# Kernel tuning notes

Measured on AMD Instinct MI355X. Metric: run time of the kernel, lower is better.

## Reference

```python
import jax, jax.numpy as jnp
import numpy as np

NEG_SLOPE = 0.2

def gatv2_layer(x, src, dst, Wl, bl, Wr, br, att, bias, N, concat):
    # Wl/Wr: [F_in, H*C]; att: [H, C]
    H, C = att.shape
    xl = (x @ Wl + bl).reshape(-1, H, C)  # source transform [N,H,C]
    xr = (x @ Wr + br).reshape(-1, H, C)  # target transform [N,H,C]
    e = jax.nn.leaky_relu(xl[src] + xr[dst], NEG_SLOPE)          # [E,H,C]
    logits = jnp.einsum('ehc,hc->eh', e, att)                    # [E,H]
    m = jax.ops.segment_max(logits, dst, num_segments=N)         # [N,H]
    p = jnp.exp(logits - m[dst])
    s = jax.ops.segment_sum(p, dst, num_segments=N)              # [N,H]
    alpha = p / s[dst]                                           # [E,H] softmax per dst
    out = jax.ops.segment_sum(alpha[:, :, None] * xl[src], dst, num_segments=N)  # [N,H,C]
    out = out.reshape(N, H * C) if concat else out.mean(axis=1)
    return out + bias


def setup_inputs() -> dict:
    key = jax.random.key(0)
    N, E, F_in = 50000, 500000, 58
    ks = jax.random.split(key, 16)
    s = 0.1
    inp = {
        'x': jax.random.normal(ks[0], (N, F_in), jnp.float32),
        'edge_index': jax.random.randint(ks[1], (2, E), 0, N, jnp.int64),
        'Wl1': jax.random.normal(ks[2], (F_in, 256), jnp.float32) * s,
        'bl1': jnp.zeros((256,), jnp.float32),
        'Wr1': jax.random.normal(ks[3], (F_in, 256), jnp.float32) * s,
        'br1': jnp.zeros((256,), jnp.float32),
        'att1': jax.random.normal(ks[4], (4, 64), jnp.float32) * s,
        'bias1': jnp.zeros((256,), jnp.float32),
        'Wl2': jax.random.normal(ks[5], (256, 256), jnp.float32) * s,
        'bl2': jnp.zeros((256,), jnp.float32),
        'Wr2': jax.random.normal(ks[6], (256, 256), jnp.float32) * s,
        'br2': jnp.zeros((256,), jnp.float32),
        'att2': jax.random.normal(ks[7], (4, 64), jnp.float32) * s,
        'bias2': jnp.zeros((256,), jnp.float32),
        'Wl3': jax.random.normal(ks[8], (256, 6), jnp.float32) * s,
        'bl3': jnp.zeros((6,), jnp.float32),
        'Wr3': jax.random.normal(ks[9], (256, 6), jnp.float32) * s,
        'br3': jnp.zeros((6,), jnp.float32),
        'att3': jax.random.normal(ks[10], (6, 1), jnp.float32) * s,
        'bias3': jnp.zeros((1,), jnp.float32),
    }
    return inp


def reference(x, edge_index, Wl1, bl1, Wr1, br1, att1, bias1,
              Wl2, bl2, Wr2, br2, att2, bias2,
              Wl3, bl3, Wr3, br3, att3, bias3):
    N = x.shape[0]
    loop = jnp.arange(N, dtype=edge_index.dtype)
    src = jnp.concatenate([edge_index[0], loop])  # self-loops (PyG default)
    dst = jnp.concatenate([edge_index[1], loop])
    h = jax.nn.elu(gatv2_layer(x, src, dst, Wl1, bl1, Wr1, br1, att1, bias1, N, True))
    h = jax.nn.elu(gatv2_layer(h, src, dst, Wl2, bl2, Wr2, br2, att2, bias2, N, True))
    out = gatv2_layer(h, src, dst, Wl3, bl3, Wr3, br3, att3, bias3, N, False)
    return out  # [N, 1]
```

## Files before the change

### kernel.cpp

```cpp
#include <hip/hip_runtime.h>
#include <math.h>

#define NEG_SLOPE 0.2f
#define LOG2E 1.4426950408889634f

typedef __attribute__((ext_vector_type(2))) _Float16 h2;
typedef __attribute__((ext_vector_type(4))) _Float16 h4;
typedef __attribute__((ext_vector_type(8))) _Float16 f16x8;
typedef __attribute__((ext_vector_type(4))) float f32x4;

template<int CTRL>
__device__ __forceinline__ float dpp_add_f32(float x) {
    int y = __builtin_amdgcn_update_dpp(0, __float_as_int(x), CTRL, 0xF, 0xF, true);
    return x + __int_as_float(y);
}
__device__ __forceinline__ float rowsum16(float x) {
    x = dpp_add_f32<0xB1>(x);
    x = dpp_add_f32<0x4E>(x);
    x = dpp_add_f32<0x124>(x);
    x = dpp_add_f32<0x128>(x);
    return x;
}


__global__ __launch_bounds__(256) void k_count(const int* __restrict__ ei, int E, int Et,
                                               int* __restrict__ cnt) {
    int e = blockIdx.x * 256 + threadIdx.x;
    if (e < Et) {
        int d = (e < E) ? ei[E + e] : (e - E);
        atomicAdd(&cnt[d], 1);
    }
}

__global__ __launch_bounds__(256) void k_scan_block(const int* __restrict__ cnt,
                                                    int* __restrict__ out,
                                                    int* __restrict__ bsums, int n) {
    __shared__ int tmp[256];
    int t = threadIdx.x;
    int i = blockIdx.x * 256 + t;
    int v = (i < n) ? cnt[i] : 0;
    tmp[t] = v;
    __syncthreads();
    for (int d = 1; d < 256; d <<= 1) {
        int add = (t >= d) ? tmp[t - d] : 0;
        __syncthreads();
        tmp[t] += add;
        __syncthreads();
    }
    if (i < n) out[i] = tmp[t] - v;
    if (t == 255) bsums[blockIdx.x] = tmp[t];
}

__global__ __launch_bounds__(256) void k_scan_bsums(int* bsums, int nb) {
    __shared__ int tmp[256];
    int t = threadIdx.x;
    int v = (t < nb) ? bsums[t] : 0;
    tmp[t] = v;
    __syncthreads();
    for (int d = 1; d < 256; d <<= 1) {
        int add = (t >= d) ? tmp[t - d] : 0;
        __syncthreads();
        tmp[t] += add;
        __syncthreads();
    }
    if (t < nb) bsums[t] = tmp[t] - v;
}

__global__ __launch_bounds__(256) void k_scan_add(int* __restrict__ out,
                                                  const int* __restrict__ bsums,
                                                  int* __restrict__ cursor,
                                                  int n, int total) {
    int i = blockIdx.x * 256 + threadIdx.x;
    if (i < n) {
        int v = out[i] + bsums[blockIdx.x];
        out[i] = v;
        cursor[i] = v;
    }
    if (i == 0) out[n] = total;
}

__global__ __launch_bounds__(256) void k_scatter(const int* __restrict__ ei, int E, int Et,
                                                 int* __restrict__ cursor,
                                                 int* __restrict__ src_sorted) {
    int e = blockIdx.x * 256 + threadIdx.x;
    if (e < Et) {
        int s, d;
        if (e < E) { s = ei[e]; d = ei[E + e]; } else { s = d = e - E; }
        int pos = atomicAdd(&cursor[d], 1);
        src_sorted[pos] = s;
    }
}


__global__ __launch_bounds__(256) void k_cast_x(const float* __restrict__ x,
                                                _Float16* __restrict__ xb,
                                                int N, int F, int kshift) {
    int i = blockIdx.x * 256 + threadIdx.x;
    if (i < (N << kshift)) {
        int n = i >> kshift, k = i & ((1 << kshift) - 1);
        float v = (k < F) ? x[n * F + k] : 0.0f;
        xb[i] = (_Float16)v;
    }
}

__global__ __launch_bounds__(256) void k_cast_w_all(
        const float* __restrict__ Wl1, const float* __restrict__ Wr1,
        const float* __restrict__ Wl2, const float* __restrict__ Wr2,
        const float* __restrict__ Wl3, const float* __restrict__ Wr3,
        _Float16* __restrict__ wtl1, _Float16* __restrict__ wtr1,
        _Float16* __restrict__ wtl2, _Float16* __restrict__ wtr2,
        _Float16* __restrict__ w3t, int F) {
    int i = blockIdx.x * 256 + threadIdx.x;
    if (i < 32768) {
        const float* W = (i < 16384) ? Wl1 : Wr1;
        _Float16* O = (i < 16384) ? wtl1 : wtr1;
        int loc = i & 16383;
        int n = loc >> 6, k = loc & 63;
        O[loc] = (_Float16)(k < F ? W[k * 256 + n] : 0.0f);
    } else if (i < 163840) {
        int seg = i - 32768;
        const float* W = (seg < 65536) ? Wl2 : Wr2;
        _Float16* O = (seg < 65536) ? wtl2 : wtr2;
        int loc = seg & 65535;
        int n = loc >> 8, k = loc & 255;
        O[loc] = (_Float16)W[k * 256 + n];
    } else if (i < 167936) {
        int loc = i - 163840;
        int j = loc >> 8, k = loc & 255;
        float v = (j < 6) ? Wl3[k * 6 + j] : ((j < 12) ? Wr3[k * 6 + (j - 6)] : 0.0f);
        w3t[loc] = (_Float16)v;
    }
}


__global__ __launch_bounds__(256) void k_gemm_pair_mfma(
        const _Float16* __restrict__ A, int M, int Kp,
        const _Float16* __restrict__ Btl, const _Float16* __restrict__ Btr,
        const float* __restrict__ bl, const float* __restrict__ br,
        _Float16* __restrict__ Cl, _Float16* __restrict__ Cr) {
    const int wave = threadIdx.x >> 6, lane = threadIdx.x & 63;
    const int l15 = lane & 15, l4 = lane >> 4;
    const int row0 = blockIdx.x * 64;
    const int mat  = wave >> 1;
    const int col0 = blockIdx.y * 128 + (wave & 1) * 64;
    const _Float16* Bt = mat ? Btr : Btl;
    const float* bias  = mat ? br  : bl;
    _Float16* C        = mat ? Cr  : Cl;

    f32x4 acc[4][4];
    #pragma unroll
    for (int a = 0; a < 4; a++)
        #pragma unroll
        for (int b = 0; b < 4; b++)
            acc[a][b] = (f32x4){0.f, 0.f, 0.f, 0.f};

    int xrow[4];
    #pragma unroll
    for (int nt = 0; nt < 4; nt++) xrow[nt] = min(row0 + nt * 16 + l15, M - 1);
    const _Float16* wbase = Bt + (size_t)(col0 + l15) * Kp + l4 * 8;
    const _Float16* xbase = A + l4 * 8;

    for (int k0 = 0; k0 < Kp; k0 += 32) {
        f16x8 wf[4], xf[4];
        #pragma unroll
        for (int ct = 0; ct < 4; ct++)
            wf[ct] = *(const f16x8*)(wbase + (size_t)(ct * 16) * Kp + k0);
        #pragma unroll
        for (int nt = 0; nt < 4; nt++)
            xf[nt] = *(const f16x8*)(xbase + (size_t)xrow[nt] * Kp + k0);
        #pragma unroll
        for (int ct = 0; ct < 4; ct++)
            #pragma unroll
            for (int nt = 0; nt < 4; nt++)
                acc[ct][nt] = __builtin_amdgcn_mfma_f32_16x16x32_f16(
                    wf[ct], xf[nt], acc[ct][nt], 0, 0, 0);
    }

    float4 bv[4];
    #pragma unroll
    for (int ct = 0; ct < 4; ct++)
        bv[ct] = *(const float4*)&bias[col0 + ct * 16 + l4 * 4];
    #pragma unroll
    for (int nt = 0; nt < 4; nt++) {
        int node = row0 + nt * 16 + l15;
        if (node < M) {
            #pragma unroll
            for (int ct = 0; ct < 4; ct++) {
                h4 hv = {(_Float16)(acc[ct][nt][0] + bv[ct].x),
                         (_Float16)(acc[ct][nt][1] + bv[ct].y),
                         (_Float16)(acc[ct][nt][2] + bv[ct].z),
                         (_Float16)(acc[ct][nt][3] + bv[ct].w)};
                *(h4*)&C[(size_t)node * 256 + col0 + ct * 16 + l4 * 4] = hv;
            }
        }
    }
}


__global__ __launch_bounds__(256) void k_gemm3_mfma(
        const _Float16* __restrict__ h,
        const _Float16* __restrict__ W3t,
        const float* __restrict__ bl, const float* __restrict__ br,
        _Float16* __restrict__ l3, int N) {
    const int wave = threadIdx.x >> 6, lane = threadIdx.x & 63;
    const int l15 = lane & 15, l4 = lane >> 4;
    const int row0 = blockIdx.x * 64 + wave * 16;
    if (row0 >= N) return;

    f16x8 bfr[8];
    #pragma unroll
    for (int ks = 0; ks < 8; ks++)
        bfr[ks] = *(const f16x8*)&W3t[l15 * 256 + ks * 32 + l4 * 8];

    const int arow = min(row0 + l15, N - 1);
    const size_t abase = (size_t)arow * 256;
    f32x4 acc = (f32x4){0.f, 0.f, 0.f, 0.f};
    #pragma unroll
    for (int ks = 0; ks < 8; ks++) {
        f16x8 af = *(const f16x8*)&h[abase + ks * 32 + l4 * 8];
        acc = __builtin_amdgcn_mfma_f32_16x16x32_f16(af, bfr[ks], acc, 0, 0, 0);
    }
    const float bv = (l15 < 6) ? bl[l15] : ((l15 < 12) ? br[l15 - 6] : 0.0f);
    #pragma unroll
    for (int r = 0; r < 4; r++) {
        int gr = row0 + l4 * 4 + r;
        if (gr < N && l15 < 12)
            l3[(size_t)gr * 16 + l15] = (_Float16)(acc[r] + bv);
    }
}


__global__ __launch_bounds__(256) void k_agg256(const _Float16* __restrict__ xl,
                                                const _Float16* __restrict__ xr,
                                                const int* __restrict__ row_ptr,
                                                const int* __restrict__ src_sorted,
                                                const float* __restrict__ att,
                                                const float* __restrict__ bias,
                                                _Float16* __restrict__ h_out, int N) {
    const int wave = threadIdx.x >> 6;
    const int lane = threadIdx.x & 63;
    const int n = __builtin_amdgcn_readfirstlane(blockIdx.x * 4 + wave);
    if (n >= N) return;
    const int ci = lane * 4;
    const h4 xr4 = *(const h4*)&xr[(size_t)n * 256 + ci];
    const float4 at4 = *(const float4*)&att[ci];
    const h2 ata = {(_Float16)(at4.x * LOG2E), (_Float16)(at4.y * LOG2E)};
    const h2 atb = {(_Float16)(at4.z * LOG2E), (_Float16)(at4.w * LOG2E)};
    float a0 = 0.f, a1 = 0.f, a2 = 0.f, a3 = 0.f;
    float m = -INFINITY, s = 0.0f;
    const int beg = row_ptr[n], end = row_ptr[n + 1];

    int j = beg;
    h4 v[8], vn[8];
    bool has = (j + 8 <= end);
    if (has) {
        #pragma unroll
        for (int e = 0; e < 8; e++) {
            int sv = src_sorted[j + e];
            v[e] = *(const h4*)&xl[(size_t)sv * 256 + ci];
        }
    }
    while (has) {
        const int jn = j + 8;
        const bool hasN = (jn + 8 <= end);
        if (hasN) {
            #pragma unroll
            for (int e = 0; e < 8; e++) {
                int sv = src_sorted[jn + e];
                vn[e] = *(const h4*)&xl[(size_t)sv * 256 + ci];
            }
        }
        float lg[8];
        #pragma unroll
        for (int e = 0; e < 8; e++) {
            h4 t = v[e] + xr4;
            h4 lk = __builtin_elementwise_max(t, t * (_Float16)NEG_SLOPE);
            h2 lo = __builtin_shufflevector(lk, lk, 0, 1);
            h2 hi = __builtin_shufflevector(lk, lk, 2, 3);
            lg[e] = __builtin_amdgcn_fdot2(lo, ata,
                        __builtin_amdgcn_fdot2(hi, atb, 0.0f, false), false);
        }
        #pragma unroll
        for (int e = 0; e < 8; e++) lg[e] = rowsum16(lg[e]);
        float bm = fmaxf(fmaxf(fmaxf(lg[0], lg[1]), fmaxf(lg[2], lg[3])),
                         fmaxf(fmaxf(lg[4], lg[5]), fmaxf(lg[6], lg[7])));
        float nm = fmaxf(m, bm);
        float sc = __builtin_amdgcn_exp2f(m - nm);
        a0 *= sc; a1 *= sc; a2 *= sc; a3 *= sc;
        float ps = 0.f;
        #pragma unroll
        for (int e = 0; e < 8; e++) {
            float p = __builtin_amdgcn_exp2f(lg[e] - nm);
            ps += p;
            a0 = fmaf(p, (float)v[e].x, a0);
            a1 = fmaf(p, (float)v[e].y, a1);
            a2 = fmaf(p, (float)v[e].z, a2);
            a3 = fmaf(p, (float)v[e].w, a3);
        }
        s = s * sc + ps;
        m = nm;
        if (hasN) {
            #pragma unroll
            for (int e = 0; e < 8; e++) v[e] = vn[e];
        }
        j = jn;
        has = hasN;
    }
    for (; j < end; j++) {
        int sv = src_sorted[j];
        h4 vv = *(const h4*)&xl[(size_t)sv * 256 + ci];
        h4 t = vv + xr4;
        h4 lk = __builtin_elementwise_max(t, t * (_Float16)NEG_SLOPE);
        h2 lo = __builtin_shufflevector(lk, lk, 0, 1);
        h2 hi = __builtin_shufflevector(lk, lk, 2, 3);
        float lg = __builtin_amdgcn_fdot2(lo, ata,
                       __builtin_amdgcn_fdot2(hi, atb, 0.0f, false), false);
        lg = rowsum16(lg);
        float nm = fmaxf(m, lg);
        float sc = __builtin_amdgcn_exp2f(m - nm);
        float p  = __builtin_amdgcn_exp2f(lg - nm);
        a0 = fmaf(p, (float)vv.x, a0 * sc);
        a1 = fmaf(p, (float)vv.y, a1 * sc);
        a2 = fmaf(p, (float)vv.z, a2 * sc);
        a3 = fmaf(p, (float)vv.w, a3 * sc);
        s = s * sc + p;
        m = nm;
    }
    const float inv = 1.0f / s;
    const float4 bv = *(const float4*)&bias[ci];
    float o0 = a0 * inv + bv.x;
    float o1 = a1 * inv + bv.y;
    float o2 = a2 * inv + bv.z;
    float o3 = a3 * inv + bv.w;
    o0 = o0 > 0.f ? o0 : (__expf(o0) - 1.f);
    o1 = o1 > 0.f ? o1 : (__expf(o1) - 1.f);
    o2 = o2 > 0.f ? o2 : (__expf(o2) - 1.f);
    o3 = o3 > 0.f ? o3 : (__expf(o3) - 1.f);
    h4 hv = {(_Float16)o0, (_Float16)o1, (_Float16)o2, (_Float16)o3};
    *(h4*)&h_out[(size_t)n * 256 + ci] = hv;
}


__global__ __launch_bounds__(64) void k_agg3(const _Float16* __restrict__ l3,
                                             const int* __restrict__ row_ptr,
                                             const int* __restrict__ src_sorted,
                                             const float* __restrict__ att3,
                                             const float* __restrict__ bias3,
                                             float* __restrict__ out, int N) {
    int n = blockIdx.x * 64 + threadIdx.x;
    if (n >= N) return;
    const h4* pn = (const h4*)&l3[(size_t)n * 16];
    h4 q1 = pn[1], q2 = pn[2];
    float xrv[6];
    xrv[0] = (float)q1.z; xrv[1] = (float)q1.w;
    xrv[2] = (float)q2.x; xrv[3] = (float)q2.y;
    xrv[4] = (float)q2.z; xrv[5] = (float)q2.w;
    float attv[6], m[6], s[6], acc[6];
    #pragma unroll
    for (int k = 0; k < 6; k++) {
        attv[k] = att3[k] * LOG2E;
        m[k] = -INFINITY; s[k] = 0.0f; acc[k] = 0.0f;
    }
    int beg = row_ptr[n], end = row_ptr[n + 1];
    for (int idx = beg; idx < end; idx++) {
        int sv = src_sorted[idx];
        const h4* ps = (const h4*)&l3[(size_t)sv * 16];
        h4 u0 = ps[0], u1 = ps[1];
        float xlv[6];
        xlv[0] = (float)u0.x; xlv[1] = (float)u0.y;
        xlv[2] = (float)u0.z; xlv[3] = (float)u0.w;
        xlv[4] = (float)u1.x; xlv[5] = (float)u1.y;
        #pragma unroll
        for (int k = 0; k < 6; k++) {
            float tt = xlv[k] + xrv[k];
            float lr = fmaxf(tt, NEG_SLOPE * tt);
            float logit = attv[k] * lr;
            float nm = fmaxf(m[k], logit);
            float sc = __builtin_amdgcn_exp2f(m[k] - nm);
            float p  = __builtin_amdgcn_exp2f(logit - nm);
            acc[k] = acc[k] * sc + p * xlv[k];
            s[k]   = s[k] * sc + p;
            m[k]   = nm;
        }
    }
    float o = 0.0f;
    #pragma unroll
    for (int k = 0; k < 6; k++) o += acc[k] / s[k];
    out[n] = o * (1.0f / 6.0f) + bias3[0];
}


extern "C" void kernel_launch(void* const* d_in, const int* in_sizes, int n_in,
                              void* d_out, int out_size, void* d_ws, size_t ws_size,
                              hipStream_t stream) {
    const float* x    = (const float*)d_in[0];
    const int*   ei   = (const int*)  d_in[1];
    const float* Wl1  = (const float*)d_in[2];
    const float* bl1  = (const float*)d_in[3];
    const float* Wr1  = (const float*)d_in[4];
    const float* br1  = (const float*)d_in[5];
    const float* att1 = (const float*)d_in[6];
    const float* bias1= (const float*)d_in[7];
    const float* Wl2  = (const float*)d_in[8];
    const float* bl2  = (const float*)d_in[9];
    const float* Wr2  = (const float*)d_in[10];
    const float* br2  = (const float*)d_in[11];
    const float* att2 = (const float*)d_in[12];
    const float* bias2= (const float*)d_in[13];
    const float* Wl3  = (const float*)d_in[14];
    const float* bl3  = (const float*)d_in[15];
    const float* Wr3  = (const float*)d_in[16];
    const float* br3  = (const float*)d_in[17];
    const float* att3 = (const float*)d_in[18];
    const float* bias3= (const float*)d_in[19];

    const int F  = in_sizes[2] / 256;
    const int N  = in_sizes[0] / F;
    const int E  = in_sizes[1] / 2;
    const int Et = E + N;

    char* ws = (char*)d_ws;
    size_t off = 0;
    auto carve = [&](size_t bytes) -> char* {
        char* p = ws + off;
        off = (off + bytes + 255) & ~(size_t)255;
        return p;
    };
    _Float16* xb   = (_Float16*)carve((size_t)N * 64 * 2);
    _Float16* xlb  = (_Float16*)carve((size_t)N * 256 * 2);
    _Float16* xrb  = (_Float16*)carve((size_t)N * 256 * 2);
    _Float16* hb   = (_Float16*)carve((size_t)N * 256 * 2);
    _Float16* wtl1 = (_Float16*)carve(256 * 64 * 2);
    _Float16* wtr1 = (_Float16*)carve(256 * 64 * 2);
    _Float16* wtl2 = (_Float16*)carve(256 * 256 * 2);
    _Float16* wtr2 = (_Float16*)carve(256 * 256 * 2);
    _Float16* w3t  = (_Float16*)carve(16 * 256 * 2);
    _Float16* l3   = (_Float16*)carve((size_t)N * 16 * 2);
    int* cnt        = (int*)carve((size_t)N * 4);
    int* row_ptr    = (int*)carve((size_t)(N + 1) * 4);
    int* cursor     = (int*)carve((size_t)N * 4);
    int* src_sorted = (int*)carve((size_t)Et * 4);
    int* bsums      = (int*)carve(1024 * 4);

    const int gN  = (N + 255) / 256;
    const int gEt = (Et + 255) / 256;
    const int gW  = (N + 3) / 4;

    hipMemsetAsync(cnt, 0, (size_t)N * 4, stream);
    k_count<<<gEt, 256, 0, stream>>>(ei, E, Et, cnt);
    k_scan_block<<<gN, 256, 0, stream>>>(cnt, row_ptr, bsums, N);
    k_scan_bsums<<<1, 256, 0, stream>>>(bsums, gN);
    k_scan_add<<<gN, 256, 0, stream>>>(row_ptr, bsums, cursor, N, Et);
    k_scatter<<<gEt, 256, 0, stream>>>(ei, E, Et, cursor, src_sorted);

    k_cast_x<<<((N << 6) + 255) / 256, 256, 0, stream>>>(x, xb, N, F, 6);
    k_cast_w_all<<<656, 256, 0, stream>>>(Wl1, Wr1, Wl2, Wr2, Wl3, Wr3,
                                          wtl1, wtr1, wtl2, wtr2, w3t, F);

    dim3 gemm_grid((N + 63) / 64, 2);

    k_gemm_pair_mfma<<<gemm_grid, 256, 0, stream>>>(xb, N, 64, wtl1, wtr1, bl1, br1, xlb, xrb);
    k_agg256<<<gW, 256, 0, stream>>>(xlb, xrb, row_ptr, src_sorted, att1, bias1, hb, N);

    k_gemm_pair_mfma<<<gemm_grid, 256, 0, stream>>>(hb, N, 256, wtl2, wtr2, bl2, br2, xlb, xrb);
    k_agg256<<<gW, 256, 0, stream>>>(xlb, xrb, row_ptr, src_sorted, att2, bias2, hb, N);

    k_gemm3_mfma<<<(N + 63) / 64, 256, 0, stream>>>(hb, w3t, bl3, br3, l3, N);
    k_agg3<<<(N + 63) / 64, 64, 0, stream>>>(l3, row_ptr, src_sorted, att3, bias3,
                                             (float*)d_out, N);
}
```

Baseline: 363.8 us.

## Stage GEMM tiles in LDS via global_load_lds with 128x128 block tiles

The paired-projection GEMM now loads 128x32 A and B tiles into shared memory using direct global-to-LDS loads, and each wave reads its fragments from LDS. Each block computes a 128x128 tile of one matrix (grid now 4 in y), so A rows are shared by two waves and B columns by two waves, instead of every wave reading its operands from global memory. It is meant to cut redundant global and L2 traffic in the GEMM. In exchange it adds two barriers per K step with no double buffering, and the LDS fragment reads may hit bank conflicts.

```diff
diff --git a/kernel.cpp b/kernel.cpp
--- a/kernel.cpp
+++ b/kernel.cpp
@@ -8,6 +8,11 @@
 typedef __attribute__((ext_vector_type(4))) _Float16 h4;
 typedef __attribute__((ext_vector_type(8))) _Float16 f16x8;
 typedef __attribute__((ext_vector_type(4))) float f32x4;
+
+typedef const __attribute__((address_space(1))) unsigned int* gu32p;
+typedef __attribute__((address_space(3))) unsigned int* lu32p;
+
+#define GLD16(g, l) __builtin_amdgcn_global_load_lds((gu32p)(g), (lu32p)(l), 16, 0, 0)
 
 template<int CTRL>
 __device__ __forceinline__ float dpp_add_f32(float x) {
@@ -138,15 +143,29 @@
         const _Float16* __restrict__ Btl, const _Float16* __restrict__ Btr,
         const float* __restrict__ bl, const float* __restrict__ br,
         _Float16* __restrict__ Cl, _Float16* __restrict__ Cr) {
-    const int wave = threadIdx.x >> 6, lane = threadIdx.x & 63;
+    __shared__ _Float16 As[128 * 32];
+    __shared__ _Float16 Bs[128 * 32];
+    const int wv = threadIdx.x >> 6, lane = threadIdx.x & 63;
+    const int wr = wv >> 1, wc = wv & 1;
     const int l15 = lane & 15, l4 = lane >> 4;
-    const int row0 = blockIdx.x * 64;
-    const int mat  = wave >> 1;
-    const int col0 = blockIdx.y * 128 + (wave & 1) * 64;
+    const int row0 = blockIdx.x * 128;
+    const int mat  = blockIdx.y >> 1;
+    const int col0 = (blockIdx.y & 1) * 128;
     const _Float16* Bt = mat ? Btr : Btl;
     const float* bias  = mat ? br  : bl;
     _Float16* C        = mat ? Cr  : Cl;
 
+    const int rl = lane >> 2;
+    const int kq = (lane & 3) * 8;
+    const _Float16* ga0 = A + (size_t)min(row0 + wv * 32 + rl,      M - 1) * Kp + kq;
+    const _Float16* ga1 = A + (size_t)min(row0 + wv * 32 + 16 + rl, M - 1) * Kp + kq;
+    const _Float16* gb0 = Bt + (size_t)(col0 + wv * 32 + rl) * Kp + kq;
+    const _Float16* gb1 = Bt + (size_t)(col0 + wv * 32 + 16 + rl) * Kp + kq;
+    _Float16* la0 = &As[(wv * 32) * 32];
+    _Float16* la1 = &As[(wv * 32 + 16) * 32];
+    _Float16* lb0 = &Bs[(wv * 32) * 32];
+    _Float16* lb1 = &Bs[(wv * 32 + 16) * 32];
+
     f32x4 acc[4][4];
     #pragma unroll
     for (int a = 0; a < 4; a++)
@@ -154,35 +173,35 @@
         for (int b = 0; b < 4; b++)
             acc[a][b] = (f32x4){0.f, 0.f, 0.f, 0.f};
 
-    int xrow[4];
-    #pragma unroll
-    for (int nt = 0; nt < 4; nt++) xrow[nt] = min(row0 + nt * 16 + l15, M - 1);
-    const _Float16* wbase = Bt + (size_t)(col0 + l15) * Kp + l4 * 8;
-    const _Float16* xbase = A + l4 * 8;
-
     for (int k0 = 0; k0 < Kp; k0 += 32) {
+        GLD16(ga0 + k0, la0);
+        GLD16(ga1 + k0, la1);
+        GLD16(gb0 + k0, lb0);
+        GLD16(gb1 + k0, lb1);
+        __syncthreads();
         f16x8 wf[4], xf[4];
         #pragma unroll
         for (int ct = 0; ct < 4; ct++)
-            wf[ct] = *(const f16x8*)(wbase + (size_t)(ct * 16) * Kp + k0);
+            wf[ct] = *(const f16x8*)&Bs[(wc * 64 + ct * 16 + l15) * 32 + l4 * 8];
         #pragma unroll
         for (int nt = 0; nt < 4; nt++)
-            xf[nt] = *(const f16x8*)(xbase + (size_t)xrow[nt] * Kp + k0);
+            xf[nt] = *(const f16x8*)&As[(wr * 64 + nt * 16 + l15) * 32 + l4 * 8];
         #pragma unroll
         for (int ct = 0; ct < 4; ct++)
             #pragma unroll
             for (int nt = 0; nt < 4; nt++)
                 acc[ct][nt] = __builtin_amdgcn_mfma_f32_16x16x32_f16(
                     wf[ct], xf[nt], acc[ct][nt], 0, 0, 0);
+        __syncthreads();
     }
 
     float4 bv[4];
     #pragma unroll
     for (int ct = 0; ct < 4; ct++)
-        bv[ct] = *(const float4*)&bias[col0 + ct * 16 + l4 * 4];
+        bv[ct] = *(const float4*)&bias[col0 + wc * 64 + ct * 16 + l4 * 4];
     #pragma unroll
     for (int nt = 0; nt < 4; nt++) {
-        int node = row0 + nt * 16 + l15;
+        int node = row0 + wr * 64 + nt * 16 + l15;
         if (node < M) {
             #pragma unroll
             for (int ct = 0; ct < 4; ct++) {
@@ -190,7 +209,7 @@
                          (_Float16)(acc[ct][nt][1] + bv[ct].y),
                          (_Float16)(acc[ct][nt][2] + bv[ct].z),
                          (_Float16)(acc[ct][nt][3] + bv[ct].w)};
-                *(h4*)&C[(size_t)node * 256 + col0 + ct * 16 + l4 * 4] = hv;
+                *(h4*)&C[(size_t)node * 256 + col0 + wc * 64 + ct * 16 + l4 * 4] = hv;
             }
         }
     }
@@ -457,7 +476,7 @@
     k_cast_w_all<<<656, 256, 0, stream>>>(Wl1, Wr1, Wl2, Wr2, Wl3, Wr3,
                                           wtl1, wtr1, wtl2, wtr2, w3t, F);
 
-    dim3 gemm_grid((N + 63) / 64, 2);
+    dim3 gemm_grid((N + 127) / 128, 4);
 
     k_gemm_pair_mfma<<<gemm_grid, 256, 0, stream>>>(xb, N, 64, wtl1, wtr1, bl1, br1, xlb, xrb);
     k_agg256<<<gW, 256, 0, stream>>>(xlb, xrb, row_ptr, src_sorted, att1, bias1, hb, N);
```

Measured after the change: 334.4 us. 1.09x faster.
